# Performance work log

Measured on AMD Instinct MI355X. Metric: run time of the kernel, lower is better.

Reference implementation:

```python
import jax, jax.numpy as jnp
import numpy as np

KSIZE = 13
DIL = 3
NUM_HEADS = 4
LN_EPS = 1e-5


def _na_idx(L, k, d):
    # NATTEN-style dilated neighborhood indices along one axis.
    i = jnp.arange(L)
    g, ii = i % d, i // d                       # dilation group, index within group
    Lg = (L - g + d - 1) // d                   # group length per position
    start = jnp.clip(ii - k // 2, 0, Lg - k)    # clamped window start (group coords)
    offs = jnp.arange(k)
    nbr = g[:, None] + d * (start[:, None] + offs[None, :])           # (L,k) absolute idx
    rel = start[:, None] + offs[None, :] - ii[:, None] + (k - 1)      # (L,k) rpb index in [0,2k-2]
    return nbr, rel


def _layernorm(x, g, b):
    mu = jnp.mean(x, -1, keepdims=True)
    var = jnp.mean(jnp.square(x - mu), -1, keepdims=True)
    return (x - mu) * jax.lax.rsqrt(var + LN_EPS) * g + b


def setup_inputs() -> dict:
    key = jax.random.key(0)
    ks = jax.random.split(key, 12)
    B, H, W, C = 1, 96, 96, 64
    mh = int(C * 4.0)
    s = 0.02
    return {
        "x": jax.random.normal(ks[0], (B, H * W, C), jnp.float32),
        "norm1_g": jnp.ones((C,), jnp.float32),
        "norm1_b": jnp.zeros((C,), jnp.float32),
        "qkv_w": jax.random.normal(ks[1], (C, 3 * C), jnp.float32) * s,
        "qkv_b": jnp.zeros((3 * C,), jnp.float32),
        "rpb": jax.random.normal(ks[2], (NUM_HEADS, 2 * KSIZE - 1, 2 * KSIZE - 1), jnp.float32) * s,
        "proj_w": jax.random.normal(ks[3], (C, C), jnp.float32) * s,
        "proj_b": jnp.zeros((C,), jnp.float32),
        "norm2_g": jnp.ones((C,), jnp.float32),
        "norm2_b": jnp.zeros((C,), jnp.float32),
        "fc1_w": jax.random.normal(ks[4], (C, mh), jnp.float32) * s,
        "fc1_b": jnp.zeros((mh,), jnp.float32),
        "fc2_w": jax.random.normal(ks[5], (mh, C), jnp.float32) * s,
        "fc2_b": jnp.zeros((C,), jnp.float32),
        "H": H,
        "W": W,
    }


def _ga(h, qkv_w, qkv_b, rpb, proj_w, proj_b):
    # h: (B,H,W,C) -> dilated neighborhood attention, kernel=13, dilation=3
    B, H, W, C = h.shape
    nh, hd = NUM_HEADS, C // NUM_HEADS
    scale = hd ** -0.5
    qkv = (h @ qkv_w + qkv_b).reshape(B, H, W, 3, nh, hd)
    qkv = qkv.transpose(3, 0, 4, 1, 2, 5)       # (3,B,nh,H,W,hd)
    q, k, v = qkv[0] * scale, qkv[1], qkv[2]
    idx_h, rel_h = _na_idx(H, KSIZE, DIL)
    idx_w, rel_w = _na_idx(W, KSIZE, DIL)
    Kk = KSIZE

    def gather(t):  # (B,nh,H,W,hd) -> (B,nh,H,W,Kk*Kk,hd)
        t = jnp.take(t, idx_h, axis=2)          # (B,nh,H,Kk,W,hd)
        t = jnp.take(t, idx_w, axis=4)          # (B,nh,H,Kk,W,Kk,hd)
        return t.transpose(0, 1, 2, 4, 3, 5, 6).reshape(B, nh, H, W, Kk * Kk, hd)

    kg = gather(k)
    vg = gather(v)
    logits = jnp.einsum('bnhwc,bnhwkc->bnhwk', q, kg)
    bias = rpb[:, rel_h]                         # (nh,H,Kk,2K-1)
    bias = bias[:, :, :, rel_w]                  # (nh,H,Kk,W,Kk)
    bias = bias.transpose(0, 1, 3, 2, 4).reshape(nh, H, W, Kk * Kk)
    attn = jax.nn.softmax(logits + bias[None], axis=-1)
    out = jnp.einsum('bnhwk,bnhwkc->bnhwc', attn, vg)
    out = out.transpose(0, 2, 3, 1, 4).reshape(B, H, W, C)
    return out @ proj_w + proj_b


def reference(x, norm1_g, norm1_b, qkv_w, qkv_b, rpb, proj_w, proj_b,
              norm2_g, norm2_b, fc1_w, fc1_b, fc2_w, fc2_b, H, W):
    B, N, C = x.shape
    shortcut = x
    h = _layernorm(x, norm1_g, norm1_b).reshape(B, H, W, C)
    h = _ga(h, qkv_w, qkv_b, rpb, proj_w, proj_b).reshape(B, N, C)
    x = shortcut + h
    h2 = _layernorm(x, norm2_g, norm2_b)
    mlp = jax.nn.gelu(h2 @ fc1_w + fc1_b, approximate=False) @ fc2_w + fc2_b
    return x + mlp
```

## Files before the change

### kernel.cpp

```cpp
#include <hip/hip_runtime.h>
#include <math.h>

#define HH 96
#define WW 96
#define CC 64
#define NH 4
#define HD 16
#define KS 13
#define KK (KS*KS)
#define NTOK (HH*WW)

__global__ __launch_bounds__(256) void ln_kernel(const float* __restrict__ x,
                                                 const float* __restrict__ g,
                                                 const float* __restrict__ b,
                                                 float* __restrict__ out) {
    int wave = threadIdx.x >> 6;
    int lane = threadIdx.x & 63;
    int token = blockIdx.x * 4 + wave;
    float v = x[token * CC + lane];
    float s = v;
    #pragma unroll
    for (int o = 1; o < 64; o <<= 1) s += __shfl_xor(s, o);
    float mu = s * (1.0f / 64.0f);
    float d = v - mu;
    float s2 = d * d;
    #pragma unroll
    for (int o = 1; o < 64; o <<= 1) s2 += __shfl_xor(s2, o);
    float var = s2 * (1.0f / 64.0f);
    out[token * CC + lane] = d * rsqrtf(var + 1e-5f) * g[lane] + b[lane];
}

template<int K, int NC, bool GELU_ACT, bool RESID, bool QSCALE>
__global__ __launch_bounds__(256) void gemm_kernel(const float* __restrict__ A,
                                                   const float* __restrict__ W,
                                                   const float* __restrict__ bias,
                                                   const float* __restrict__ resid,
                                                   float* __restrict__ out) {
    __shared__ float Ast[K][34];
    const int t0 = blockIdx.x * 32;
    const int tc = threadIdx.x & 15;
    const int tr = threadIdx.x >> 4;
    const int r0 = tr * 2;
    const int c  = blockIdx.y * 64 + tc * 4;

    for (int i = threadIdx.x; i < 32 * K; i += 256) {
        int r = i / K, cc = i % K;
        Ast[cc][r] = A[t0 * K + i];
    }
    __syncthreads();

    float4 b4 = *(const float4*)&bias[c];
    float4 acc0 = b4, acc1 = b4;
    #pragma unroll 8
    for (int k = 0; k < K; k++) {
        float2 a = *(const float2*)&Ast[k][r0];
        float4 w = *(const float4*)&W[k * NC + c];
        acc0.x += a.x * w.x; acc0.y += a.x * w.y; acc0.z += a.x * w.z; acc0.w += a.x * w.w;
        acc1.x += a.y * w.x; acc1.y += a.y * w.y; acc1.z += a.y * w.z; acc1.w += a.y * w.w;
    }

    if (QSCALE && blockIdx.y == 0) {
        acc0.x *= 0.25f; acc0.y *= 0.25f; acc0.z *= 0.25f; acc0.w *= 0.25f;
        acc1.x *= 0.25f; acc1.y *= 0.25f; acc1.z *= 0.25f; acc1.w *= 0.25f;
    }
    if (GELU_ACT) {
        #define GELU1(v) v = 0.5f * v * (1.0f + erff(v * 0.70710678118f))
        GELU1(acc0.x); GELU1(acc0.y); GELU1(acc0.z); GELU1(acc0.w);
        GELU1(acc1.x); GELU1(acc1.y); GELU1(acc1.z); GELU1(acc1.w);
        #undef GELU1
    }
    if (RESID) {
        float4 r0v = *(const float4*)&resid[(t0 + r0) * NC + c];
        float4 r1v = *(const float4*)&resid[(t0 + r0 + 1) * NC + c];
        acc0.x += r0v.x; acc0.y += r0v.y; acc0.z += r0v.z; acc0.w += r0v.w;
        acc1.x += r1v.x; acc1.y += r1v.y; acc1.z += r1v.z; acc1.w += r1v.w;
    }
    *(float4*)&out[(t0 + r0) * NC + c] = acc0;
    *(float4*)&out[(t0 + r0 + 1) * NC + c] = acc1;
}

__device__ __forceinline__ float dpp_reduce16(float p) {
    int t;
    t = __builtin_amdgcn_update_dpp(0, __float_as_int(p), 0xB1, 0xF, 0xF, true);
    p += __int_as_float(t);
    t = __builtin_amdgcn_update_dpp(0, __float_as_int(p), 0x4E, 0xF, 0xF, true);
    p += __int_as_float(t);
    t = __builtin_amdgcn_update_dpp(0, __float_as_int(p), 0x141, 0xF, 0xF, true);
    p += __int_as_float(t);
    t = __builtin_amdgcn_update_dpp(0, __float_as_int(p), 0x140, 0xF, 0xF, true);
    p += __int_as_float(t);
    return p;
}

__global__ __launch_bounds__(256) void na_attn_kernel(const float* __restrict__ qkv,
                                                      const float* __restrict__ rpb,
                                                      float* __restrict__ out) {
    int wave = threadIdx.x >> 6;
    int lane = threadIdx.x & 63;
    int token = blockIdx.x * 4 + wave;
    int head = lane >> 4;
    int dim  = lane & 15;

    int y = token / WW, x = token - y * WW;
    int gh = y % 3, ih = y / 3;
    int gw = x % 3, iw = x / 3;
    int sh = ih - 6; sh = sh < 0 ? 0 : (sh > 19 ? 19 : sh);
    int sw = iw - 6; sw = sw < 0 ? 0 : (sw > 19 ? 19 : sw);

    int co = head * HD + dim;
    float q = qkv[token * 192 + co];
    const float* bias_h = rpb + head * 625 + (sw - iw + 12);

    float acc = 0.0f, s = 0.0f;
    for (int kh = 0; kh < KS; kh++) {
        int ny = gh + 3 * (sh + kh);
        int rh = sh + kh - ih + 12;
        const float* kp = qkv + (ny * WW + gw + 3 * sw) * 192 + 64 + co;
        const float* bp = bias_h + rh * 25;
        #pragma unroll
        for (int kw = 0; kw < KS; kw++) {
            float kv = kp[kw * 576];
            float vv = kp[kw * 576 + 64];
            float p = dpp_reduce16(q * kv);
            float e = __expf(p + bp[kw]);
            s += e;
            acc += e * vv;
        }
    }
    out[token * CC + co] = acc / s;
}

extern "C" void kernel_launch(void* const* d_in, const int* in_sizes, int n_in,
                              void* d_out, int out_size, void* d_ws, size_t ws_size,
                              hipStream_t stream) {
    const float* x       = (const float*)d_in[0];
    const float* norm1_g = (const float*)d_in[1];
    const float* norm1_b = (const float*)d_in[2];
    const float* qkv_w   = (const float*)d_in[3];
    const float* qkv_b   = (const float*)d_in[4];
    const float* rpb     = (const float*)d_in[5];
    const float* proj_w  = (const float*)d_in[6];
    const float* proj_b  = (const float*)d_in[7];
    const float* norm2_g = (const float*)d_in[8];
    const float* norm2_b = (const float*)d_in[9];
    const float* fc1_w   = (const float*)d_in[10];
    const float* fc1_b   = (const float*)d_in[11];
    const float* fc2_w   = (const float*)d_in[12];
    const float* fc2_b   = (const float*)d_in[13];
    float* out = (float*)d_out;

    float* ws = (float*)d_ws;
    float* h1       = ws;
    float* qkv      = h1 + NTOK * CC;
    float* attn_out = qkv + NTOK * 192;
    float* x2       = attn_out + NTOK * CC;
    float* h2       = x2 + NTOK * CC;
    float* hidden   = h2 + NTOK * CC;

    dim3 blk(256);
    ln_kernel<<<NTOK / 4, blk, 0, stream>>>(x, norm1_g, norm1_b, h1);
    gemm_kernel<64, 192, false, false, true><<<dim3(NTOK / 32, 3), blk, 0, stream>>>(h1, qkv_w, qkv_b, nullptr, qkv);
    na_attn_kernel<<<NTOK / 4, blk, 0, stream>>>(qkv, rpb, attn_out);
    gemm_kernel<64, 64, false, true, false><<<dim3(NTOK / 32, 1), blk, 0, stream>>>(attn_out, proj_w, proj_b, x, x2);
    ln_kernel<<<NTOK / 4, blk, 0, stream>>>(x2, norm2_g, norm2_b, h2);
    gemm_kernel<64, 256, true, false, false><<<dim3(NTOK / 32, 4), blk, 0, stream>>>(h2, fc1_w, fc1_b, nullptr, hidden);
    gemm_kernel<256, 64, false, true, false><<<dim3(NTOK / 32, 1), blk, 0, stream>>>(hidden, fc2_w, fc2_b, x2, out);
}
```

Before: 186.0 us.

## Fuse layernorms into GEMMs and merge proj/LN2/MLP into one kernel

Folds the first layernorm into the QKV GEMM prologue, operating on the shared-memory tile. It also merges the projection, residual add, second layernorm, fc1+GELU and fc2+residual into one per-32-token-tile kernel, with intermediates kept in LDS. This removes four kernel launches and the global round-trips for h1, x2, h2 and the 256-wide hidden activation. In exchange, the fused MLP kernel uses about 47KB of LDS and many accumulator registers, which lowers occupancy, and it launches only 288 blocks.

```diff
diff --git a/kernel.cpp b/kernel.cpp
--- a/kernel.cpp
+++ b/kernel.cpp
@@ -10,86 +10,83 @@
 #define KK (KS*KS)
 #define NTOK (HH*WW)
 
-__global__ __launch_bounds__(256) void ln_kernel(const float* __restrict__ x,
-                                                 const float* __restrict__ g,
-                                                 const float* __restrict__ b,
-                                                 float* __restrict__ out) {
-    int wave = threadIdx.x >> 6;
-    int lane = threadIdx.x & 63;
-    int token = blockIdx.x * 4 + wave;
-    float v = x[token * CC + lane];
-    float s = v;
-    #pragma unroll
-    for (int o = 1; o < 64; o <<= 1) s += __shfl_xor(s, o);
+__device__ __forceinline__ float dpp_reduce8(float p) {
+    int t;
+    t = __builtin_amdgcn_update_dpp(0, __float_as_int(p), 0xB1, 0xF, 0xF, true);
+    p += __int_as_float(t);
+    t = __builtin_amdgcn_update_dpp(0, __float_as_int(p), 0x4E, 0xF, 0xF, true);
+    p += __int_as_float(t);
+    t = __builtin_amdgcn_update_dpp(0, __float_as_int(p), 0x141, 0xF, 0xF, true);
+    p += __int_as_float(t);
+    return p;
+}
+__device__ __forceinline__ float dpp_reduce16(float p) {
+    p = dpp_reduce8(p);
+    int t = __builtin_amdgcn_update_dpp(0, __float_as_int(p), 0x140, 0xF, 0xF, true);
+    p += __int_as_float(t);
+    return p;
+}
+
+__device__ __forceinline__ void ln_rows32(float (*buf)[34],
+                                          const float* __restrict__ g,
+                                          const float* __restrict__ b,
+                                          int tid) {
+    int r  = tid >> 3;
+    int c0 = (tid & 7) * 8;
+    float v[8];
+    float s = 0.0f;
+    #pragma unroll
+    for (int j = 0; j < 8; j++) { v[j] = buf[c0 + j][r]; s += v[j]; }
+    s = dpp_reduce8(s);
     float mu = s * (1.0f / 64.0f);
-    float d = v - mu;
-    float s2 = d * d;
-    #pragma unroll
-    for (int o = 1; o < 64; o <<= 1) s2 += __shfl_xor(s2, o);
-    float var = s2 * (1.0f / 64.0f);
-    out[token * CC + lane] = d * rsqrtf(var + 1e-5f) * g[lane] + b[lane];
-}
-
-template<int K, int NC, bool GELU_ACT, bool RESID, bool QSCALE>
-__global__ __launch_bounds__(256) void gemm_kernel(const float* __restrict__ A,
-                                                   const float* __restrict__ W,
-                                                   const float* __restrict__ bias,
-                                                   const float* __restrict__ resid,
-                                                   float* __restrict__ out) {
-    __shared__ float Ast[K][34];
+    float s2 = 0.0f;
+    #pragma unroll
+    for (int j = 0; j < 8; j++) { float d = v[j] - mu; s2 += d * d; }
+    s2 = dpp_reduce8(s2);
+    float inv = rsqrtf(s2 * (1.0f / 64.0f) + 1e-5f);
+    #pragma unroll
+    for (int j = 0; j < 8; j++)
+        buf[c0 + j][r] = (v[j] - mu) * inv * g[c0 + j] + b[c0 + j];
+}
+
+__global__ __launch_bounds__(256) void ln_gemm_kernel(const float* __restrict__ x,
+                                                      const float* __restrict__ g,
+                                                      const float* __restrict__ b,
+                                                      const float* __restrict__ W,
+                                                      const float* __restrict__ bias,
+                                                      float* __restrict__ out) {
+    __shared__ float Ast[64][34];
     const int t0 = blockIdx.x * 32;
-    const int tc = threadIdx.x & 15;
-    const int tr = threadIdx.x >> 4;
+    const int tid = threadIdx.x;
+
+    for (int i = tid; i < 32 * 64; i += 256) {
+        int r = i >> 6, cc = i & 63;
+        Ast[cc][r] = x[t0 * 64 + i];
+    }
+    __syncthreads();
+    ln_rows32(Ast, g, b, tid);
+    __syncthreads();
+
+    const int tc = tid & 15;
+    const int tr = tid >> 4;
     const int r0 = tr * 2;
     const int c  = blockIdx.y * 64 + tc * 4;
-
-    for (int i = threadIdx.x; i < 32 * K; i += 256) {
-        int r = i / K, cc = i % K;
-        Ast[cc][r] = A[t0 * K + i];
-    }
-    __syncthreads();
 
     float4 b4 = *(const float4*)&bias[c];
     float4 acc0 = b4, acc1 = b4;
     #pragma unroll 8
-    for (int k = 0; k < K; k++) {
+    for (int k = 0; k < 64; k++) {
         float2 a = *(const float2*)&Ast[k][r0];
-        float4 w = *(const float4*)&W[k * NC + c];
+        float4 w = *(const float4*)&W[k * 192 + c];
         acc0.x += a.x * w.x; acc0.y += a.x * w.y; acc0.z += a.x * w.z; acc0.w += a.x * w.w;
         acc1.x += a.y * w.x; acc1.y += a.y * w.y; acc1.z += a.y * w.z; acc1.w += a.y * w.w;
     }
-
-    if (QSCALE && blockIdx.y == 0) {
+    if (blockIdx.y == 0) {
         acc0.x *= 0.25f; acc0.y *= 0.25f; acc0.z *= 0.25f; acc0.w *= 0.25f;
         acc1.x *= 0.25f; acc1.y *= 0.25f; acc1.z *= 0.25f; acc1.w *= 0.25f;
     }
-    if (GELU_ACT) {
-        #define GELU1(v) v = 0.5f * v * (1.0f + erff(v * 0.70710678118f))
-        GELU1(acc0.x); GELU1(acc0.y); GELU1(acc0.z); GELU1(acc0.w);
-        GELU1(acc1.x); GELU1(acc1.y); GELU1(acc1.z); GELU1(acc1.w);
-        #undef GELU1
-    }
-    if (RESID) {
-        float4 r0v = *(const float4*)&resid[(t0 + r0) * NC + c];
-        float4 r1v = *(const float4*)&resid[(t0 + r0 + 1) * NC + c];
-        acc0.x += r0v.x; acc0.y += r0v.y; acc0.z += r0v.z; acc0.w += r0v.w;
-        acc1.x += r1v.x; acc1.y += r1v.y; acc1.z += r1v.z; acc1.w += r1v.w;
-    }
-    *(float4*)&out[(t0 + r0) * NC + c] = acc0;
-    *(float4*)&out[(t0 + r0 + 1) * NC + c] = acc1;
-}
-
-__device__ __forceinline__ float dpp_reduce16(float p) {
-    int t;
-    t = __builtin_amdgcn_update_dpp(0, __float_as_int(p), 0xB1, 0xF, 0xF, true);
-    p += __int_as_float(t);
-    t = __builtin_amdgcn_update_dpp(0, __float_as_int(p), 0x4E, 0xF, 0xF, true);
-    p += __int_as_float(t);
-    t = __builtin_amdgcn_update_dpp(0, __float_as_int(p), 0x141, 0xF, 0xF, true);
-    p += __int_as_float(t);
-    t = __builtin_amdgcn_update_dpp(0, __float_as_int(p), 0x140, 0xF, 0xF, true);
-    p += __int_as_float(t);
-    return p;
+    *(float4*)&out[(t0 + r0) * 192 + c] = acc0;
+    *(float4*)&out[(t0 + r0 + 1) * 192 + c] = acc1;
 }
 
 __global__ __launch_bounds__(256) void na_attn_kernel(const float* __restrict__ qkv,
@@ -128,6 +125,105 @@
         }
     }
     out[token * CC + co] = acc / s;
+}
+
+__global__ __launch_bounds__(256) void mlp_fused_kernel(const float* __restrict__ attn_out,
+                                                        const float* __restrict__ x,
+                                                        const float* __restrict__ proj_w,
+                                                        const float* __restrict__ proj_b,
+                                                        const float* __restrict__ n2g,
+                                                        const float* __restrict__ n2b,
+                                                        const float* __restrict__ fc1_w,
+                                                        const float* __restrict__ fc1_b,
+                                                        const float* __restrict__ fc2_w,
+                                                        const float* __restrict__ fc2_b,
+                                                        float* __restrict__ out) {
+    __shared__ float Ast[64][34];
+    __shared__ float X2T[64][34];
+    __shared__ float Hid[256][34];
+
+    const int t0 = blockIdx.x * 32;
+    const int tid = threadIdx.x;
+
+    for (int i = tid; i < 32 * 64; i += 256) {
+        int r = i >> 6, cc = i & 63;
+        Ast[cc][r] = attn_out[t0 * 64 + i];
+    }
+    __syncthreads();
+
+    const int tc = tid & 15;
+    const int tr = tid >> 4;
+    const int r0 = tr * 2;
+    const int c  = tc * 4;
+
+    float4 pb = *(const float4*)&proj_b[c];
+    float4 a0 = pb, a1 = pb;
+    #pragma unroll 8
+    for (int k = 0; k < 64; k++) {
+        float2 a = *(const float2*)&Ast[k][r0];
+        float4 w = *(const float4*)&proj_w[k * 64 + c];
+        a0.x += a.x * w.x; a0.y += a.x * w.y; a0.z += a.x * w.z; a0.w += a.x * w.w;
+        a1.x += a.y * w.x; a1.y += a.y * w.y; a1.z += a.y * w.z; a1.w += a.y * w.w;
+    }
+    {
+        float4 x0 = *(const float4*)&x[(t0 + r0) * 64 + c];
+        float4 x1 = *(const float4*)&x[(t0 + r0 + 1) * 64 + c];
+        a0.x += x0.x; a0.y += x0.y; a0.z += x0.z; a0.w += x0.w;
+        a1.x += x1.x; a1.y += x1.y; a1.z += x1.z; a1.w += x1.w;
+    }
+    X2T[c + 0][r0] = a0.x; X2T[c + 1][r0] = a0.y; X2T[c + 2][r0] = a0.z; X2T[c + 3][r0] = a0.w;
+    X2T[c + 0][r0 + 1] = a1.x; X2T[c + 1][r0 + 1] = a1.y; X2T[c + 2][r0 + 1] = a1.z; X2T[c + 3][r0 + 1] = a1.w;
+    __syncthreads();
+
+    ln_rows32(X2T, n2g, n2b, tid);
+    __syncthreads();
+
+    float4 h0[4], h1[4];
+    #pragma unroll
+    for (int gg = 0; gg < 4; gg++) {
+        float4 bb = *(const float4*)&fc1_b[c + gg * 64];
+        h0[gg] = bb; h1[gg] = bb;
+    }
+    #pragma unroll 4
+    for (int k = 0; k < 64; k++) {
+        float2 a = *(const float2*)&X2T[k][r0];
+        #pragma unroll
+        for (int gg = 0; gg < 4; gg++) {
+            float4 w = *(const float4*)&fc1_w[k * 256 + c + gg * 64];
+            h0[gg].x += a.x * w.x; h0[gg].y += a.x * w.y; h0[gg].z += a.x * w.z; h0[gg].w += a.x * w.w;
+            h1[gg].x += a.y * w.x; h1[gg].y += a.y * w.y; h1[gg].z += a.y * w.z; h1[gg].w += a.y * w.w;
+        }
+    }
+    #define GELU1(v) v = 0.5f * v * (1.0f + erff(v * 0.70710678118f))
+    #pragma unroll
+    for (int gg = 0; gg < 4; gg++) {
+        GELU1(h0[gg].x); GELU1(h0[gg].y); GELU1(h0[gg].z); GELU1(h0[gg].w);
+        GELU1(h1[gg].x); GELU1(h1[gg].y); GELU1(h1[gg].z); GELU1(h1[gg].w);
+    }
+    #undef GELU1
+    #pragma unroll
+    for (int gg = 0; gg < 4; gg++) {
+        int col = c + gg * 64;
+        Hid[col + 0][r0] = h0[gg].x; Hid[col + 1][r0] = h0[gg].y;
+        Hid[col + 2][r0] = h0[gg].z; Hid[col + 3][r0] = h0[gg].w;
+        Hid[col + 0][r0 + 1] = h1[gg].x; Hid[col + 1][r0 + 1] = h1[gg].y;
+        Hid[col + 2][r0 + 1] = h1[gg].z; Hid[col + 3][r0 + 1] = h1[gg].w;
+    }
+    __syncthreads();
+
+    float4 ob = *(const float4*)&fc2_b[c];
+    float4 o0 = ob, o1 = ob;
+    #pragma unroll 8
+    for (int k = 0; k < 256; k++) {
+        float2 a = *(const float2*)&Hid[k][r0];
+        float4 w = *(const float4*)&fc2_w[k * 64 + c];
+        o0.x += a.x * w.x; o0.y += a.x * w.y; o0.z += a.x * w.z; o0.w += a.x * w.w;
+        o1.x += a.y * w.x; o1.y += a.y * w.y; o1.z += a.y * w.z; o1.w += a.y * w.w;
+    }
+    o0.x += a0.x; o0.y += a0.y; o0.z += a0.z; o0.w += a0.w;
+    o1.x += a1.x; o1.y += a1.y; o1.z += a1.z; o1.w += a1.w;
+    *(float4*)&out[(t0 + r0) * 64 + c] = o0;
+    *(float4*)&out[(t0 + r0 + 1) * 64 + c] = o1;
 }
 
 extern "C" void kernel_launch(void* const* d_in, const int* in_sizes, int n_in,
@@ -150,19 +246,13 @@
     float* out = (float*)d_out;
 
     float* ws = (float*)d_ws;
-    float* h1       = ws;
-    float* qkv      = h1 + NTOK * CC;
+    float* qkv      = ws;
     float* attn_out = qkv + NTOK * 192;
-    float* x2       = attn_out + NTOK * CC;
-    float* h2       = x2 + NTOK * CC;
-    float* hidden   = h2 + NTOK * CC;
 
     dim3 blk(256);
-    ln_kernel<<<NTOK / 4, blk, 0, stream>>>(x, norm1_g, norm1_b, h1);
-    gemm_kernel<64, 192, false, false, true><<<dim3(NTOK / 32, 3), blk, 0, stream>>>(h1, qkv_w, qkv_b, nullptr, qkv);
+    ln_gemm_kernel<<<dim3(NTOK / 32, 3), blk, 0, stream>>>(x, norm1_g, norm1_b, qkv_w, qkv_b, qkv);
     na_attn_kernel<<<NTOK / 4, blk, 0, stream>>>(qkv, rpb, attn_out);
-    gemm_kernel<64, 64, false, true, false><<<dim3(NTOK / 32, 1), blk, 0, stream>>>(attn_out, proj_w, proj_b, x, x2);
-    ln_kernel<<<NTOK / 4, blk, 0, stream>>>(x2, norm2_g, norm2_b, h2);
-    gemm_kernel<64, 256, true, false, false><<<dim3(NTOK / 32, 4), blk, 0, stream>>>(h2, fc1_w, fc1_b, nullptr, hidden);
-    gemm_kernel<256, 64, false, true, false><<<dim3(NTOK / 32, 1), blk, 0, stream>>>(hidden, fc2_w, fc2_b, x2, out);
-}
+    mlp_fused_kernel<<<NTOK / 32, blk, 0, stream>>>(attn_out, x, proj_w, proj_b,
+                                                    norm2_g, norm2_b, fc1_w, fc1_b,
+                                                    fc2_w, fc2_b, out);
+}
```

Result: faster. 177.6 us (-4.5%).
